# Kernel optimization log

Hardware: AMD Instinct MI355X
Metric: run time of the kernel (lower is better)

## Reference

```python
import jax, jax.numpy as jnp
import numpy as np

L, H, T, C, OUT, B = 8, 16, 2048, 1024, 1024, 4
DH = C // H
EPS = 1e-5


def _sincos_pos_embed(embed_dim, n):
    omega = np.arange(embed_dim // 2, dtype=np.float64) / (embed_dim / 2.0)
    omega = 1.0 / 10000 ** omega
    out = np.einsum('m,d->md', np.arange(n, dtype=np.float64), omega)
    return np.concatenate([np.sin(out), np.cos(out)], axis=1).astype(np.float32)


def setup_inputs() -> dict:
    key = jax.random.key(0)
    ks = jax.random.split(key, 12)
    s = 0.02  # torch init std
    n = lambda k, sh: jax.random.normal(k, sh, jnp.float32) * s
    zc = jnp.zeros((L, C), jnp.float32)
    return {
        'seq': jax.random.normal(ks[0], (B, T, C), jnp.float32),
        'pos_embed': jnp.asarray(_sincos_pos_embed(C, T))[None],  # [1,T,C]
        'Wq': n(ks[1], (L, C, C)), 'bq': zc,
        'Wk': n(ks[2], (L, C, C)), 'bk': zc,
        'Wv': n(ks[3], (L, C, C)), 'bv': zc,
        'Wo': n(ks[4], (L, C, C)), 'bo': zc,
        'ln1_w': jnp.ones((L, C), jnp.float32), 'ln1_b': zc,
        'ln2_w': jnp.ones((L, C), jnp.float32), 'ln2_b': zc,
        'W1': n(ks[5], (L, 4 * C, C)), 'b1': jnp.zeros((L, 4 * C), jnp.float32),
        'W2': n(ks[6], (L, C, 4 * C)), 'b2': zc,
        'lnf_w': jnp.ones((C,), jnp.float32), 'lnf_b': jnp.zeros((C,), jnp.float32),
        'Whead': n(ks[7], (OUT, C)),
    }


def _ln(x, w, b):
    mu = jnp.mean(x, -1, keepdims=True)
    var = jnp.mean(jnp.square(x - mu), -1, keepdims=True)
    return (x - mu) * jax.lax.rsqrt(var + EPS) * w + b


def _block(x, p):
    (Wq, bq, Wk, bk, Wv, bv, Wo, bo, l1w, l1b, l2w, l2b, W1, b1, W2, b2) = p
    b_, t_, c_ = x.shape
    h = _ln(x, l1w, l1b)
    q = (h @ Wq.T + bq).reshape(b_, t_, H, DH)
    k = (h @ Wk.T + bk).reshape(b_, t_, H, DH)
    v = (h @ Wv.T + bv).reshape(b_, t_, H, DH)
    # NOTE: source mask buffer is all ones -> no masking (full softmax)
    att = jnp.einsum('bqhd,bkhd->bhqk', q, k) * (1.0 / np.sqrt(DH))
    att = jax.nn.softmax(att, axis=-1)
    y = jnp.einsum('bhqk,bkhd->bqhd', att, v).reshape(b_, t_, c_)
    x = x + y @ Wo.T + bo
    h2 = _ln(x, l2w, l2b)
    x = x + jax.nn.gelu(h2 @ W1.T + b1, approximate=False) @ W2.T + b2
    return x, None


def reference(seq, pos_embed, Wq, bq, Wk, bk, Wv, bv, Wo, bo,
              ln1_w, ln1_b, ln2_w, ln2_b, W1, b1, W2, b2,
              lnf_w, lnf_b, Whead):
    t = seq.shape[1]
    x = seq + pos_embed[:, -t:, :]  # embedding dropout is identity at eval
    params = (Wq, bq, Wk, bk, Wv, bv, Wo, bo, ln1_w, ln1_b, ln2_w, ln2_b, W1, b1, W2, b2)
    x, _ = jax.lax.scan(_block, x, params)
    x = _ln(x, lnf_w, lnf_b)
    return x @ Whead.T
```

## Files before the change

### kernel.cpp

```cpp
#include <hip/hip_runtime.h>
#include <hip/hip_bf16.h>


#define LAYERS 8
#define NH 16
#define TT 2048
#define CC 1024
#define NB 4
#define MR (NB*TT)
#define LN_EPS 1e-5f

typedef __bf16 bf16_t;
typedef __attribute__((ext_vector_type(8))) __bf16 bf16x8;
typedef __attribute__((ext_vector_type(4))) __bf16 bf16x4;
typedef __attribute__((ext_vector_type(4))) float f32x4;
typedef __attribute__((ext_vector_type(8))) short s16x8;
typedef __attribute__((ext_vector_type(4))) unsigned u32x4;

__device__ inline f32x4 mfma16x16x32(bf16x8 a, bf16x8 b, f32x4 c) {
    return __builtin_amdgcn_mfma_f32_16x16x32_bf16(a, b, c, 0, 0, 0);
}

__device__ inline void gload_lds16(const void* g, void* lds) {
    __builtin_amdgcn_global_load_lds((const __attribute__((address_space(1))) void*)g,
                                     (__attribute__((address_space(3))) void*)lds, 16, 0, 0);
}

__device__ inline unsigned pack_bf16(float a, float b) {
    unsigned short ua = __builtin_bit_cast(unsigned short, (bf16_t)a);
    unsigned short ub = __builtin_bit_cast(unsigned short, (bf16_t)b);
    return (unsigned)ua | ((unsigned)ub << 16);
}


__global__ __launch_bounds__(256) void add_pos_k(const float* __restrict__ s,
                                                 const float* __restrict__ p,
                                                 float* __restrict__ x) {
    int i = blockIdx.x * 256 + threadIdx.x;
    float4 a = ((const float4*)s)[i];
    float4 b = ((const float4*)p)[i & ((TT * CC / 4) - 1)];
    ((float4*)x)[i] = make_float4(a.x + b.x, a.y + b.y, a.z + b.z, a.w + b.w);
}

__global__ __launch_bounds__(256) void f32_to_bf16_k(const float* __restrict__ s,
                                                     bf16_t* __restrict__ d, int n4) {
    int i = blockIdx.x * 256 + threadIdx.x;
    if (i < n4) {
        float4 v = ((const float4*)s)[i];
        bf16x4 o;
        o[0] = (bf16_t)v.x; o[1] = (bf16_t)v.y; o[2] = (bf16_t)v.z; o[3] = (bf16_t)v.w;
        ((bf16x4*)d)[i] = o;
    }
}

__global__ __launch_bounds__(256) void convert_layer_k(
        const float* __restrict__ Wq, const float* __restrict__ Wk,
        const float* __restrict__ Wv, const float* __restrict__ Wo,
        const float* __restrict__ W1, const float* __restrict__ W2,
        const float* __restrict__ bq, const float* __restrict__ bk,
        const float* __restrict__ bv,
        bf16_t* __restrict__ wqkvb, bf16_t* __restrict__ wob,
        bf16_t* __restrict__ w1b, bf16_t* __restrict__ w2b,
        float* __restrict__ bqkv) {
    const int i = blockIdx.x * 256 + threadIdx.x;
    if (i < 3145728) {
        const float4* s4;
        bf16_t* dst;
        int off;
        if (i < 262144)       { s4 = (const float4*)Wq + i;             dst = wqkvb; off = i; }
        else if (i < 524288)  { s4 = (const float4*)Wk + (i - 262144);  dst = wqkvb; off = i; }
        else if (i < 786432)  { s4 = (const float4*)Wv + (i - 524288);  dst = wqkvb; off = i; }
        else if (i < 1048576) { s4 = (const float4*)Wo + (i - 786432);  dst = wob;   off = i - 786432; }
        else if (i < 2097152) { s4 = (const float4*)W1 + (i - 1048576); dst = w1b;   off = i - 1048576; }
        else                  { s4 = (const float4*)W2 + (i - 2097152); dst = w2b;   off = i - 2097152; }
        float4 v = *s4;
        bf16x4 o;
        o[0] = (bf16_t)v.x; o[1] = (bf16_t)v.y; o[2] = (bf16_t)v.z; o[3] = (bf16_t)v.w;
        ((bf16x4*)dst)[off] = o;
    } else if (i < 3146496) {
        const int j = i - 3145728;
        const float* b = (j < 256) ? bq : (j < 512 ? bk : bv);
        ((float4*)bqkv)[j] = ((const float4*)b)[j & 255];
    }
}


__global__ __launch_bounds__(256) void ln_rows_k(const float* __restrict__ x,
                                                 const float* __restrict__ wgt,
                                                 const float* __restrict__ bgt,
                                                 bf16_t* __restrict__ out) {
    const int row = blockIdx.x * 4 + (threadIdx.x >> 6);
    const int l = threadIdx.x & 63;
    const float* xr = x + (size_t)row * CC;
    float4 v[4];
    float s = 0.f, sq = 0.f;
#pragma unroll
    for (int j = 0; j < 4; j++) {
        v[j] = *(const float4*)&xr[j * 256 + l * 4];
        s  += v[j].x + v[j].y + v[j].z + v[j].w;
        sq += v[j].x * v[j].x + v[j].y * v[j].y + v[j].z * v[j].z + v[j].w * v[j].w;
    }
#pragma unroll
    for (int m = 1; m < 64; m <<= 1) { s += __shfl_xor(s, m); sq += __shfl_xor(sq, m); }
    const float mu = s * (1.f / CC);
    const float rstd = rsqrtf(sq * (1.f / CC) - mu * mu + LN_EPS);
#pragma unroll
    for (int j = 0; j < 4; j++) {
        const int c0 = j * 256 + l * 4;
        const float4 wv = *(const float4*)&wgt[c0];
        const float4 bv = *(const float4*)&bgt[c0];
        bf16x4 o;
        o[0] = (bf16_t)((v[j].x - mu) * rstd * wv.x + bv.x);
        o[1] = (bf16_t)((v[j].y - mu) * rstd * wv.y + bv.y);
        o[2] = (bf16_t)((v[j].z - mu) * rstd * wv.z + bv.z);
        o[3] = (bf16_t)((v[j].w - mu) * rstd * wv.w + bv.w);
        *(bf16x4*)&out[(size_t)row * CC + c0] = o;
    }
}


#define EPI_BF16 0
#define EPI_GELU 1
#define EPI_RES  2
#define EPI_F32  3

template <int EPI>
__global__ __launch_bounds__(256) void gemm_bt(const bf16_t* __restrict__ A,
                                               const bf16_t* __restrict__ Bw,
                                               const float* __restrict__ bias,
                                               float* __restrict__ resid,
                                               bf16_t* __restrict__ obf,
                                               float* __restrict__ of32,
                                               int N, int K, int nbn) {
    __shared__ __align__(16) bf16_t As[128 * 32];
    __shared__ __align__(16) bf16_t Bs[128 * 32];
    const int nwg = gridDim.x;
    const int id = blockIdx.x;
    const int swz = (id & 7) * (nwg >> 3) + (id >> 3);
    const int bn = swz % nbn, bm = swz / nbn;
    const int t = threadIdx.x, w = t >> 6, l = t & 63;
    const int wm = (w >> 1) << 6, wn = (w & 1) << 6;
    const int fr = l & 15, fg = l >> 4;
    const int srow = l >> 2, scol = (l & 3) * 8;
    f32x4 acc[4][4] = {};
    for (int k0 = 0; k0 < K; k0 += 32) {
#pragma unroll
        for (int it = 0; it < 2; ++it) {
            const int rr = it * 64 + w * 16;
            gload_lds16(A  + (size_t)(bm * 128 + rr + srow) * K + k0 + scol, &As[rr * 32]);
            gload_lds16(Bw + (size_t)(bn * 128 + rr + srow) * K + k0 + scol, &Bs[rr * 32]);
        }
        __syncthreads();
        bf16x8 af[4], bfv[4];
#pragma unroll
        for (int i = 0; i < 4; i++) af[i]  = *(const bf16x8*)&As[(wm + i * 16 + fr) * 32 + fg * 8];
#pragma unroll
        for (int j = 0; j < 4; j++) bfv[j] = *(const bf16x8*)&Bs[(wn + j * 16 + fr) * 32 + fg * 8];
#pragma unroll
        for (int i = 0; i < 4; i++)
#pragma unroll
            for (int j = 0; j < 4; j++)
                acc[i][j] = mfma16x16x32(af[i], bfv[j], acc[i][j]);
        __syncthreads();
    }
#pragma unroll
    for (int i = 0; i < 4; i++) {
#pragma unroll
        for (int j = 0; j < 4; j++) {
            const int col = bn * 128 + wn + j * 16 + fr;
            float bv = 0.f;
            if constexpr (EPI != EPI_F32) bv = bias[col];
#pragma unroll
            for (int rg = 0; rg < 4; ++rg) {
                const int row = bm * 128 + wm + i * 16 + fg * 4 + rg;
                float v = acc[i][j][rg] + bv;
                if constexpr (EPI == EPI_BF16) {
                    obf[(size_t)row * N + col] = (bf16_t)v;
                } else if constexpr (EPI == EPI_GELU) {
                    v = 0.5f * v * (1.0f + erff(v * 0.70710678118f));
                    obf[(size_t)row * N + col] = (bf16_t)v;
                } else if constexpr (EPI == EPI_RES) {
                    resid[(size_t)row * CC + col] += v;
                } else {
                    of32[(size_t)row * N + col] = v;
                }
            }
        }
    }
}


__global__ __launch_bounds__(256, 4) void attn_k(const bf16_t* __restrict__ qkv,
                                                 bf16_t* __restrict__ y) {
    __shared__ __align__(16) bf16_t Ks[64 * 64];
    __shared__ __align__(16) bf16_t Vt[64 * 64];
    const int id = blockIdx.x;
    const int swz = (id & 7) * 256 + (id >> 3);
    const int qt = swz & 31, bh = swz >> 5;
    const int b = bh >> 4, h = bh & 15;
    const int t = threadIdx.x, w = t >> 6, l = t & 63;
    const int fr = l & 15, fg = l >> 4;
    const int hh = fg >> 1;
    const int q0 = qt * 64 + w * 16;
    const size_t bT = (size_t)b * TT;
    const float SCL = 0.125f * 1.44269504f;

    bf16x8 qf[2];
    {
        const size_t qoff = (bT + q0 + fr) * 3072 + h * 64 + fg * 8;
        qf[0] = *(const bf16x8*)&qkv[qoff];
        qf[1] = *(const bf16x8*)&qkv[qoff + 32];
    }
    float mrun = -1e30f, lse = 0.f;
    f32x4 oacc[4] = {};

    const int srow = t >> 2;
    const int c8a = (t & 3) * 8;
    const int ksw = (srow & 7) << 4;
    char* KsB = (char*)Ks;
    char* VtB = (char*)Vt;

    s16x8 kr0, kr1, vr0, vr1;
    auto preload = [&](int kv0) {
        const size_t roff = (bT + kv0 + srow) * 3072 + h * 64;
        kr0 = *(const s16x8*)&qkv[roff + 1024 + c8a];
        kr1 = *(const s16x8*)&qkv[roff + 1024 + c8a + 32];
        vr0 = *(const s16x8*)&qkv[roff + 2048 + c8a];
        vr1 = *(const s16x8*)&qkv[roff + 2048 + c8a + 32];
    };
    preload(0);

    for (int kv0 = 0; kv0 < TT; kv0 += 64) {
        __syncthreads();
#pragma unroll
        for (int half = 0; half < 2; ++half) {
            const s16x8 kr = half ? kr1 : kr0;
            const s16x8 vr = half ? vr1 : vr0;
            const int c8 = c8a + half * 32;
            *(s16x8*)(KsB + srow * 128 + ((c8 * 2) ^ ksw)) = kr;
#pragma unroll
            for (int j = 0; j < 8; j++) {
                const int d = c8 + j;
                const int dsw = (((d & 7) ^ ((d >> 3) & 7)) << 4);
                *(short*)(VtB + d * 128 + ((srow * 2) ^ dsw)) = vr[j];
            }
        }
        __syncthreads();
        if (kv0 + 64 < TT) preload(kv0 + 64);

        f32x4 sacc[4] = {};
#pragma unroll
        for (int nt = 0; nt < 4; nt++) {
            const int kr_ = nt * 16 + fr;
            const int sw = (kr_ & 7) << 4;
#pragma unroll
            for (int c = 0; c < 2; c++) {
                bf16x8 kf = *(const bf16x8*)(KsB + kr_ * 128 + ((c * 64 + fg * 16) ^ sw));
                sacc[nt] = mfma16x16x32(kf, qf[c], sacc[nt]);
            }
        }
        float tm = sacc[0][0];
#pragma unroll
        for (int nt = 0; nt < 4; nt++)
#pragma unroll
            for (int rg = 0; rg < 4; rg++) tm = fmaxf(tm, sacc[nt][rg]);
        tm = fmaxf(tm, __shfl_xor(tm, 16));
        tm = fmaxf(tm, __shfl_xor(tm, 32));
        tm *= SCL;
        if (!__all(tm - mrun <= 11.5f)) {
            const float mn = fmaxf(mrun, tm);
            const float co = exp2f(mrun - mn);
            lse *= co; mrun = mn;
            const float cr0 = __shfl(co, fg * 4 + 0);
            const float cr1 = __shfl(co, fg * 4 + 1);
            const float cr2 = __shfl(co, fg * 4 + 2);
            const float cr3 = __shfl(co, fg * 4 + 3);
#pragma unroll
            for (int nd = 0; nd < 4; nd++) {
                oacc[nd][0] *= cr0; oacc[nd][1] *= cr1;
                oacc[nd][2] *= cr2; oacc[nd][3] *= cr3;
            }
        }
        const f32x4 sA0 = hh ? sacc[1] : sacc[0];
        const f32x4 sA1 = hh ? sacc[3] : sacc[2];
        const f32x4 sB0 = hh ? sacc[0] : sacc[1];
        const f32x4 sB1 = hh ? sacc[2] : sacc[3];
        float rs = 0.f;
        unsigned pkA[4], pkB[4];
#pragma unroll
        for (int rg = 0; rg < 4; rg++) {
            const float a0 = exp2f(sA0[rg] * SCL - mrun);
            const float a1 = exp2f(sA1[rg] * SCL - mrun);
            const float b0 = exp2f(sB0[rg] * SCL - mrun);
            const float b1 = exp2f(sB1[rg] * SCL - mrun);
            rs += (a0 + a1) + (b0 + b1);
            pkA[rg] = pack_bf16(a0, a1);
            pkB[rg] = pack_bf16(b0, b1);
        }
        rs += __shfl_xor(rs, 16);
        rs += __shfl_xor(rs, 32);
        lse += rs;
        unsigned s0pk[4], s1pk[4];
#pragma unroll
        for (int rg = 0; rg < 4; rg++) {
            const unsigned r16 = __shfl_xor(pkA[rg], 16);
            const unsigned r32 = __shfl_xor(pkB[rg], 32);
            const unsigned r48 = __shfl_xor(pkB[rg], 48);
            s0pk[rg] = (fg == 0) ? pkA[rg] : (fg == 1) ? r48 : (fg == 2) ? r32 : r16;
            s1pk[rg] = (fg == 0) ? r16 : (fg == 1) ? r32 : (fg == 2) ? r48 : pkA[rg];
        }
        u32x4 w0v, w1v;
        w0v[0] = (s0pk[0] & 0xFFFFu) | (s0pk[1] << 16);
        w0v[1] = (s0pk[2] & 0xFFFFu) | (s0pk[3] << 16);
        w0v[2] = (s1pk[0] & 0xFFFFu) | (s1pk[1] << 16);
        w0v[3] = (s1pk[2] & 0xFFFFu) | (s1pk[3] << 16);
        w1v[0] = (s0pk[0] >> 16) | (s0pk[1] & 0xFFFF0000u);
        w1v[1] = (s0pk[2] >> 16) | (s0pk[3] & 0xFFFF0000u);
        w1v[2] = (s1pk[0] >> 16) | (s1pk[1] & 0xFFFF0000u);
        w1v[3] = (s1pk[2] >> 16) | (s1pk[3] & 0xFFFF0000u);
        const bf16x8 paf0 = __builtin_bit_cast(bf16x8, w0v);
        const bf16x8 paf1 = __builtin_bit_cast(bf16x8, w1v);
#pragma unroll
        for (int nd = 0; nd < 4; nd++) {
            const int dr = nd * 16 + fr;
            const int dsw = (((dr & 7) ^ ((dr >> 3) & 7)) << 4);
            bf16x8 vf0 = *(const bf16x8*)(VtB + dr * 128 + ((fg * 16) ^ dsw));
            oacc[nd] = mfma16x16x32(paf0, vf0, oacc[nd]);
            bf16x8 vf1 = *(const bf16x8*)(VtB + dr * 128 + ((64 + fg * 16) ^ dsw));
            oacc[nd] = mfma16x16x32(paf1, vf1, oacc[nd]);
        }
    }
    const float inv = 1.f / lse;
    const float i0 = __shfl(inv, fg * 4 + 0);
    const float i1 = __shfl(inv, fg * 4 + 1);
    const float i2 = __shfl(inv, fg * 4 + 2);
    const float i3 = __shfl(inv, fg * 4 + 3);
#pragma unroll
    for (int nd = 0; nd < 4; nd++) {
        const size_t ro = (bT + q0 + fg * 4) * CC + h * 64 + nd * 16 + fr;
        y[ro]          = (bf16_t)(oacc[nd][0] * i0);
        y[ro + CC]     = (bf16_t)(oacc[nd][1] * i1);
        y[ro + 2 * CC] = (bf16_t)(oacc[nd][2] * i2);
        y[ro + 3 * CC] = (bf16_t)(oacc[nd][3] * i3);
    }
}


extern "C" void kernel_launch(void* const* d_in, const int* in_sizes, int n_in,
                              void* d_out, int out_size, void* d_ws, size_t ws_size,
                              hipStream_t stream) {
    (void)in_sizes; (void)n_in; (void)out_size; (void)ws_size;
    const float* seq  = (const float*)d_in[0];
    const float* pos  = (const float*)d_in[1];
    const float* Wq   = (const float*)d_in[2];
    const float* bq   = (const float*)d_in[3];
    const float* Wk   = (const float*)d_in[4];
    const float* bk   = (const float*)d_in[5];
    const float* Wv   = (const float*)d_in[6];
    const float* bv   = (const float*)d_in[7];
    const float* Wo   = (const float*)d_in[8];
    const float* bo   = (const float*)d_in[9];
    const float* ln1w = (const float*)d_in[10];
    const float* ln1b = (const float*)d_in[11];
    const float* ln2w = (const float*)d_in[12];
    const float* ln2b = (const float*)d_in[13];
    const float* W1   = (const float*)d_in[14];
    const float* b1   = (const float*)d_in[15];
    const float* W2   = (const float*)d_in[16];
    const float* b2   = (const float*)d_in[17];
    const float* lnfw = (const float*)d_in[18];
    const float* lnfb = (const float*)d_in[19];
    const float* Wh   = (const float*)d_in[20];
    float* out = (float*)d_out;

    char* ws = (char*)d_ws;
    float*  x     = (float*)(ws + 0);
    bf16_t* qkvb  = (bf16_t*)(ws + 33554432);
    bf16_t* yb    = (bf16_t*)(ws + 83886080);
    bf16_t* a1b   = (bf16_t*)(ws + 33554432);
    bf16_t* hb    = (bf16_t*)(ws + 100663296);
    bf16_t* wqkvb = (bf16_t*)(ws + 117440512);
    bf16_t* wob   = (bf16_t*)(ws + 123731968);
    bf16_t* w1b   = (bf16_t*)(ws + 125829120);
    bf16_t* w2b   = (bf16_t*)(ws + 134217728);
    bf16_t* whb   = (bf16_t*)(ws + 142606336);
    float*  bqkv  = (float*)(ws + 144703488);

    f32_to_bf16_k<<<1024, 256, 0, stream>>>(Wh, whb, 262144);
    add_pos_k<<<8192, 256, 0, stream>>>(seq, pos, x);

    for (int l = 0; l < LAYERS; ++l) {
        const size_t wo_ = (size_t)l * CC * CC;
        const size_t w4_ = (size_t)l * 4 * CC * CC;
        convert_layer_k<<<12291, 256, 0, stream>>>(Wq + wo_, Wk + wo_, Wv + wo_, Wo + wo_,
                                                   W1 + w4_, W2 + w4_,
                                                   bq + l * CC, bk + l * CC, bv + l * CC,
                                                   wqkvb, wob, w1b, w2b, bqkv);

        ln_rows_k<<<2048, 256, 0, stream>>>(x, ln1w + l * CC, ln1b + l * CC, hb);
        gemm_bt<EPI_BF16><<<1536, 256, 0, stream>>>(hb, wqkvb, bqkv, nullptr,
                                                    qkvb, nullptr, 3072, 1024, 24);
        attn_k<<<2048, 256, 0, stream>>>(qkvb, yb);
        gemm_bt<EPI_RES><<<512, 256, 0, stream>>>(yb, wob, bo + l * CC, x,
                                                  nullptr, nullptr, 1024, 1024, 8);
        ln_rows_k<<<2048, 256, 0, stream>>>(x, ln2w + l * CC, ln2b + l * CC, hb);
        gemm_bt<EPI_GELU><<<2048, 256, 0, stream>>>(hb, w1b, b1 + (size_t)l * 4 * CC,
                                                    nullptr, a1b, nullptr, 4096, 1024, 32);
        gemm_bt<EPI_RES><<<512, 256, 0, stream>>>(a1b, w2b, b2 + l * CC, x,
                                                  nullptr, nullptr, 1024, 4096, 8);
    }
    ln_rows_k<<<2048, 256, 0, stream>>>(x, lnfw, lnfb, hb);
    gemm_bt<EPI_F32><<<512, 256, 0, stream>>>(hb, whb, nullptr, nullptr,
                                              nullptr, out, 1024, 1024, 8);
}
```

Before: 4.620 ms.

## Add 256x256-tile 8-wave GEMM with triple-buffered LDS for QKV and FC1

Adds a new GEMM kernel with 512 threads per workgroup and a 256x256 output tile. It uses a three-stage LDS ring filled by direct global-to-LDS loads, swizzled LDS addressing, and interleaves MFMA bursts at raised wave priority with prefetch of later stages. The QKV projection and the GELU FC1 GEMMs use it instead of the 128-tile kernel, to raise arithmetic intensity and hide load latency. The trade-off is much larger LDS use, one workgroup per CU, and fewer workgroups, which may reduce occupancy and cause tail imbalance.

```diff
diff --git a/kernel.cpp b/kernel.cpp
--- a/kernel.cpp
+++ b/kernel.cpp
@@ -190,6 +190,97 @@
 }
 
 
+template <int EPI>
+__global__ __launch_bounds__(512, 1) void gemm8p(const bf16_t* __restrict__ A,
+                                                 const bf16_t* __restrict__ Bw,
+                                                 const float* __restrict__ bias,
+                                                 bf16_t* __restrict__ obf,
+                                                 int N, int K, int nbn) {
+    extern __shared__ __align__(16) char smem[];
+    bf16_t* ldsA = (bf16_t*)smem;
+    bf16_t* ldsB = (bf16_t*)smem + 24576;
+    const int nwg = gridDim.x;
+    const int id  = blockIdx.x;
+    const int swzid = (id & 7) * (nwg >> 3) + (id >> 3);
+    const int bn = swzid % nbn, bm = swzid / nbn;
+    const int t = threadIdx.x, wv = t >> 6, lane = t & 63;
+    const int fr = lane & 15, fg = lane >> 4;
+    const int wm2 = (wv >> 2) * 128, wn2 = (wv & 3) * 64;
+    const int swf = ((fr & 8) ? 16 : 0) | ((fr & 4) ? 8 : 0);
+    const int rdA0 = (wm2 + fr) * 32 + ((fg * 8) ^ swf);
+    const int rdB0 = (wn2 + fr) * 32 + ((fg * 8) ^ swf);
+    const int rr0 = wv * 16 + (lane >> 2);
+    const int sws = ((rr0 & 8) ? 16 : 0) | ((rr0 & 4) ? 8 : 0);
+    const size_t gA0 = (size_t)(bm * 256 + rr0) * K + (((lane & 3) * 8) ^ sws);
+    const size_t gB0 = (size_t)(bn * 256 + rr0) * K + (((lane & 3) * 8) ^ sws);
+    const int ldsStage = wv * 512;
+    const int NT = K >> 5;
+
+    f32x4 acc[8][4] = {};
+
+    auto stA = [&](int T) {
+        bf16_t* dst = ldsA + (T % 3) * 8192 + ldsStage;
+        const bf16_t* s = A + gA0 + (size_t)T * 32;
+        gload_lds16(s, dst);
+        gload_lds16(s + (size_t)128 * K, dst + 4096);
+    };
+    auto stB = [&](int T) {
+        bf16_t* dst = ldsB + (T % 3) * 8192 + ldsStage;
+        const bf16_t* s = Bw + gB0 + (size_t)T * 32;
+        gload_lds16(s, dst);
+        gload_lds16(s + (size_t)128 * K, dst + 4096);
+    };
+    stA(0); stB(0); stA(1); stB(1);
+
+    for (int T = 0; T < NT; ++T) {
+        if (T == NT - 1) asm volatile("s_waitcnt vmcnt(0)" ::: "memory");
+        else             asm volatile("s_waitcnt vmcnt(4)" ::: "memory");
+        __builtin_amdgcn_s_barrier();
+        const bf16_t* As_ = ldsA + (T % 3) * 8192;
+        const bf16_t* Bs_ = ldsB + (T % 3) * 8192;
+        bf16x8 af[4], bf[4];
+#pragma unroll
+        for (int i = 0; i < 4; i++) af[i] = *(const bf16x8*)&As_[rdA0 + i * 512];
+#pragma unroll
+        for (int i = 0; i < 4; i++) bf[i] = *(const bf16x8*)&Bs_[rdB0 + i * 512];
+        if (T + 2 < NT) stA(T + 2);
+        __builtin_amdgcn_s_setprio(1);
+#pragma unroll
+        for (int mi = 0; mi < 4; mi++)
+#pragma unroll
+            for (int ni = 0; ni < 4; ni++)
+                acc[mi][ni] = mfma16x16x32(af[mi], bf[ni], acc[mi][ni]);
+        __builtin_amdgcn_s_setprio(0);
+#pragma unroll
+        for (int i = 0; i < 4; i++) af[i] = *(const bf16x8*)&As_[rdA0 + (4 + i) * 512];
+        if (T + 2 < NT) stB(T + 2);
+        __builtin_amdgcn_s_setprio(1);
+#pragma unroll
+        for (int mi = 0; mi < 4; mi++)
+#pragma unroll
+            for (int ni = 0; ni < 4; ni++)
+                acc[4 + mi][ni] = mfma16x16x32(af[mi], bf[ni], acc[4 + mi][ni]);
+        __builtin_amdgcn_s_setprio(0);
+    }
+#pragma unroll
+    for (int mi = 0; mi < 8; mi++) {
+#pragma unroll
+        for (int ni = 0; ni < 4; ni++) {
+            const int col = bn * 256 + wn2 + ni * 16 + fr;
+            const float bv = bias[col];
+#pragma unroll
+            for (int rg = 0; rg < 4; rg++) {
+                const int row = bm * 256 + wm2 + mi * 16 + fg * 4 + rg;
+                float v = acc[mi][ni][rg] + bv;
+                if constexpr (EPI == EPI_GELU)
+                    v = 0.5f * v * (1.0f + erff(v * 0.70710678118f));
+                obf[(size_t)row * N + col] = (bf16_t)v;
+            }
+        }
+    }
+}
+
+
 __global__ __launch_bounds__(256, 4) void attn_k(const bf16_t* __restrict__ qkv,
                                                  bf16_t* __restrict__ y) {
     __shared__ __align__(16) bf16_t Ks[64 * 64];
@@ -386,6 +477,11 @@
     bf16_t* whb   = (bf16_t*)(ws + 142606336);
     float*  bqkv  = (float*)(ws + 144703488);
 
+    hipFuncSetAttribute(reinterpret_cast<const void*>(gemm8p<EPI_BF16>),
+                        hipFuncAttributeMaxDynamicSharedMemorySize, 98304);
+    hipFuncSetAttribute(reinterpret_cast<const void*>(gemm8p<EPI_GELU>),
+                        hipFuncAttributeMaxDynamicSharedMemorySize, 98304);
+
     f32_to_bf16_k<<<1024, 256, 0, stream>>>(Wh, whb, 262144);
     add_pos_k<<<8192, 256, 0, stream>>>(seq, pos, x);
 
@@ -398,14 +494,14 @@
                                                    wqkvb, wob, w1b, w2b, bqkv);
 
         ln_rows_k<<<2048, 256, 0, stream>>>(x, ln1w + l * CC, ln1b + l * CC, hb);
-        gemm_bt<EPI_BF16><<<1536, 256, 0, stream>>>(hb, wqkvb, bqkv, nullptr,
-                                                    qkvb, nullptr, 3072, 1024, 24);
+        gemm8p<EPI_BF16><<<384, 512, 98304, stream>>>(hb, wqkvb, bqkv, qkvb,
+                                                      3072, 1024, 12);
         attn_k<<<2048, 256, 0, stream>>>(qkvb, yb);
         gemm_bt<EPI_RES><<<512, 256, 0, stream>>>(yb, wob, bo + l * CC, x,
                                                   nullptr, nullptr, 1024, 1024, 8);
         ln_rows_k<<<2048, 256, 0, stream>>>(x, ln2w + l * CC, ln2b + l * CC, hb);
-        gemm_bt<EPI_GELU><<<2048, 256, 0, stream>>>(hb, w1b, b1 + (size_t)l * 4 * CC,
-                                                    nullptr, a1b, nullptr, 4096, 1024, 32);
+        gemm8p<EPI_GELU><<<512, 512, 98304, stream>>>(hb, w1b, b1 + (size_t)l * 4 * CC,
+                                                      a1b, 4096, 1024, 16);
         gemm_bt<EPI_RES><<<512, 256, 0, stream>>>(a1b, w2b, b2 + l * CC, x,
                                                   nullptr, nullptr, 1024, 4096, 8);
     }
```

Result: faster. 4.310 ms (-6.7%).
